# Kernel tuning notes

Hardware: AMD Instinct MI355X
Metric: run time of the kernel (lower is better)

## Reference

```python
import jax, jax.numpy as jnp
import numpy as np

OFFSET = 1
NUM_ENTITY = 128

def setup_inputs() -> dict:
    key = jax.random.key(0)
    ks = jax.random.split(key, 8)
    B, L, D = 32, 2048, 1024
    M, E, S = 256, NUM_ENTITY, 128
    H, P = 2048, 512
    return {
        "sequence_output": jax.random.normal(ks[0], (B, L, D), dtype=jnp.float32),
        "mention_pos": jax.random.randint(ks[1], (B, M), 0, L - 2),
        "mention2entity": jnp.sort(jax.random.randint(ks[2], (B, M), 0, E), axis=-1),
        "sent_pos": jax.random.randint(ks[3], (B, S), 0, L - 2),
        "fc1_w": jax.random.normal(ks[4], (D, H), dtype=jnp.float32) * 0.02,
        "fc1_b": jnp.zeros((H,), dtype=jnp.float32),
        "fc2_w": jax.random.normal(ks[5], (H, P), dtype=jnp.float32) * 0.02,
        "fc2_b": jnp.zeros((P,), dtype=jnp.float32),
    }

def _segment_logsumexp(x, seg):
    # x: [M, D] mention embeddings, seg: [M] entity ids -> [E, D]
    m = jax.ops.segment_max(x, seg, num_segments=NUM_ENTITY)           # [E, D]
    m_safe = jnp.where(jnp.isfinite(m), m, 0.0)
    s = jax.ops.segment_sum(jnp.exp(x - m_safe[seg]), seg, num_segments=NUM_ENTITY)
    cnt = jax.ops.segment_sum(jnp.ones((x.shape[0],), x.dtype), seg, num_segments=NUM_ENTITY)
    s_safe = jnp.where(cnt[:, None] > 0, s, 1.0)
    lse = jnp.log(s_safe) + m_safe
    # entities with no mentions stay zero (torch.zeros init in original)
    return jnp.where(cnt[:, None] > 0, lse, 0.0)

def reference(sequence_output, mention_pos, mention2entity, sent_pos, fc1_w, fc1_b, fc2_w, fc2_b):
    # gather mention start-token states (offset = +1 as in self.offset)
    mention_embed = jnp.take_along_axis(
        sequence_output, (mention_pos + OFFSET)[:, :, None], axis=1)  # [B, M, D]
    sent_embed = jnp.take_along_axis(
        sequence_output, (sent_pos + OFFSET)[:, :, None], axis=1)     # [B, S, D]
    entity_embed = jax.vmap(_segment_logsumexp)(mention_embed, mention2entity)  # [B, E, D]
    nodes = jnp.concatenate([mention_embed, entity_embed, sent_embed], axis=1)  # [B, M+E+S, D]
    # projection(): fc1 then fc2 (no nonlinearity, as in the original)
    h = jnp.einsum('bnd,dh->bnh', nodes, fc1_w) + fc1_b
    return jnp.einsum('bnh,hp->bnp', h, fc2_w) + fc2_b
```

## Files before the change

### kernel.cpp

```cpp
#include <hip/hip_runtime.h>
#include <cstdint>

#define DEV __device__ __forceinline__

typedef __attribute__((ext_vector_type(8))) short short8;
typedef __attribute__((ext_vector_type(4))) float f32x4;

DEV unsigned short f2bf(float f) {
    uint32_t u = __builtin_bit_cast(uint32_t, f);
    u += 0x7fffu + ((u >> 16) & 1u);
    return (unsigned short)(u >> 16);
}

DEV uint32_t cvtpk(float a, float b) {
    uint32_t r;
    asm("v_cvt_pk_bf16_f32 %0, %1, %2" : "=v"(r) : "v"(a), "v"(b));
    return r;
}

DEV uint2 pack4(float4 v) {
    uint2 o;
    o.x = cvtpk(v.x, v.y);
    o.y = cvtpk(v.z, v.w);
    return o;
}

DEV void async_copy16(void* lds, const void* g) {
    __builtin_amdgcn_global_load_lds(
        (const __attribute__((address_space(1))) void*)g,
        (__attribute__((address_space(3))) void*)lds, 16, 0, 0);
}

template <int KLEN, int KSTR, int N>
DEV void gemm_body_part(const unsigned short* __restrict__ A,
                        const unsigned short* __restrict__ Bt,
                        float* __restrict__ P,
                        int Mtot, int rowblk, int colblk, int zidx,
                        unsigned short* Al, unsigned short* Bl) {
    int t = threadIdx.x;
    int lane = t & 63, w = t >> 6;
    int wm = w >> 1, wn = w & 1;
    int row0 = rowblk * 128, col0 = colblk * 128;
    size_t kbase = (size_t)zidx * KLEN;
    f32x4 acc[4][4] = {};

    int rifc = lane >> 2;
    int koff = (lane & 3) * 8;
    int c0 = 2 * w, c1 = 2 * w + 1;

    const unsigned short* Abase = A + (size_t)row0 * KSTR + kbase + koff;
    const unsigned short* Bbase = Bt + (size_t)col0 * KSTR + kbase + koff;

    for (int kt = 0; kt < KLEN / 32; ++kt) {
        int k0 = kt * 32;
        __syncthreads();
        async_copy16(&Al[c0 * 512], Abase + (size_t)(c0 * 16 + rifc) * KSTR + k0);
        async_copy16(&Al[c1 * 512], Abase + (size_t)(c1 * 16 + rifc) * KSTR + k0);
        async_copy16(&Bl[c0 * 512], Bbase + (size_t)(c0 * 16 + rifc) * KSTR + k0);
        async_copy16(&Bl[c1 * 512], Bbase + (size_t)(c1 * 16 + rifc) * KSTR + k0);
        __syncthreads();

        int r = lane & 15, kq = lane >> 4;
        short8 a[4], b[4];
        #pragma unroll
        for (int mi = 0; mi < 4; ++mi)
            a[mi] = *reinterpret_cast<const short8*>(&Al[(wm * 64 + mi * 16 + r) * 32 + kq * 8]);
        #pragma unroll
        for (int ni = 0; ni < 4; ++ni)
            b[ni] = *reinterpret_cast<const short8*>(&Bl[(wn * 64 + ni * 16 + r) * 32 + kq * 8]);
        #pragma unroll
        for (int mi = 0; mi < 4; ++mi)
            #pragma unroll
            for (int ni = 0; ni < 4; ++ni)
                acc[mi][ni] = __builtin_amdgcn_mfma_f32_16x16x32_bf16(a[mi], b[ni], acc[mi][ni], 0, 0, 0);
    }

    int r = lane & 15, kq = lane >> 4;
    float* Pz = P + (size_t)zidx * (size_t)N * (size_t)Mtot;
    #pragma unroll
    for (int mi = 0; mi < 4; ++mi)
        #pragma unroll
        for (int ni = 0; ni < 4; ++ni) {
            int col = col0 + wn * 64 + ni * 16 + r;
            #pragma unroll
            for (int j = 0; j < 4; ++j) {
                int row = row0 + wm * 64 + mi * 16 + kq * 4 + j;
                Pz[(size_t)col * Mtot + row] = acc[mi][ni][j];
            }
        }
}

__global__ __launch_bounds__(256) void k_prep(const float* __restrict__ W1,
                                              const float* __restrict__ W2,
                                              const float* __restrict__ b1,
                                              unsigned short* __restrict__ W1c,
                                              unsigned short* __restrict__ W2t,
                                              float* __restrict__ part) {
    __shared__ unsigned short sh[32][33];
    int blk = blockIdx.x, t = threadIdx.x;
    if (blk < 2048) {
        int i = blk * 256 + t;
        float4 v = reinterpret_cast<const float4*>(W1)[i];
        reinterpret_cast<uint2*>(W1c)[i] = pack4(v);
    } else if (blk < 3072) {
        int idx = blk - 2048;
        int h0 = (idx & 63) * 32, p0 = (idx >> 6) * 32;
        int r = t >> 3, c4 = (t & 7) * 4;
        float4 v = *reinterpret_cast<const float4*>(&W2[(size_t)(h0 + r) * 512 + p0 + c4]);
        sh[r][c4 + 0] = f2bf(v.x);
        sh[r][c4 + 1] = f2bf(v.y);
        sh[r][c4 + 2] = f2bf(v.z);
        sh[r][c4 + 3] = f2bf(v.w);
        __syncthreads();
        uint2 o;
        o.x = (uint32_t)sh[c4 + 0][r] | ((uint32_t)sh[c4 + 1][r] << 16);
        o.y = (uint32_t)sh[c4 + 2][r] | ((uint32_t)sh[c4 + 3][r] << 16);
        *reinterpret_cast<uint2*>(&W2t[(size_t)(p0 + r) * 2048 + h0 + c4]) = o;
    } else {
        int hs = blk - 3072;
        float a0 = 0.f, a1 = 0.f;
        #pragma unroll 4
        for (int hh = 0; hh < 32; ++hh) {
            int h = hs * 32 + hh;
            float bb = b1[h];
            a0 += bb * W2[(size_t)h * 512 + t];
            a1 += bb * W2[(size_t)h * 512 + 256 + t];
        }
        part[hs * 512 + t] = a0;
        part[hs * 512 + 256 + t] = a1;
    }
}

__global__ __launch_bounds__(256) void k_mid(const float* __restrict__ seq,
                                             const int* __restrict__ mpos,
                                             const int* __restrict__ m2e,
                                             const unsigned short* __restrict__ W1c,
                                             const unsigned short* __restrict__ W2t,
                                             float* __restrict__ Wpart,
                                             const float* __restrict__ part,
                                             const float* __restrict__ b2,
                                             float* __restrict__ fb,
                                             unsigned short* __restrict__ ent) {
    __shared__ unsigned short Al[128 * 32];
    __shared__ unsigned short Bl[128 * 32];
    __shared__ int sm[256];
    __shared__ int sp[256];
    __shared__ int slo, shi;
    int blk = blockIdx.x, t = threadIdx.x;
    if (blk < 128) {
        gemm_body_part<512, 2048, 512>(W1c, W2t, Wpart, 1024,
                                       (blk >> 2) & 7, blk & 3, blk >> 5, Al, Bl);
    } else if (blk < 130) {
        int p = (blk - 128) * 256 + t;
        float s = b2[p];
        #pragma unroll
        for (int hs = 0; hs < 64; ++hs) s += part[hs * 512 + p];
        fb[p] = s;
    } else {
        int idx = blk - 130;
        int b = idx >> 7, e = idx & 127;
        sm[t] = m2e[b * 256 + t];
        sp[t] = mpos[b * 256 + t] + 1;
        if (t == 0) { slo = 0; shi = 0; }
        __syncthreads();
        if (sm[t] == e && (t == 0 || sm[t - 1] != e)) slo = t;
        if (sm[t] == e && (t == 255 || sm[t + 1] != e)) shi = t + 1;
        __syncthreads();
        int lo = slo, hi = shi;
        float ox, oy, oz, ow;
        if (hi > lo) {
            float s0 = 0.f, s1 = 0.f, s2 = 0.f, s3 = 0.f;
            for (int j = lo; j < hi; ++j) {
                float4 v = *reinterpret_cast<const float4*>(
                    &seq[((size_t)b * 2048 + sp[j]) * 1024 + t * 4]);
                s0 += __expf(v.x); s1 += __expf(v.y);
                s2 += __expf(v.z); s3 += __expf(v.w);
            }
            ox = __logf(s0); oy = __logf(s1);
            oz = __logf(s2); ow = __logf(s3);
        } else {
            ox = oy = oz = ow = 0.f;
        }
        float4 o; o.x = ox; o.y = oy; o.z = oz; o.w = ow;
        *reinterpret_cast<uint2*>(&ent[((size_t)b * 128 + e) * 1024 + t * 4]) = pack4(o);
    }
}

__global__ __launch_bounds__(256) void k_wreduce(const float* __restrict__ P,
                                                 unsigned short* __restrict__ Wt) {
    const size_t SPLIT = 512u * 1024u;
    int i = blockIdx.x * 256 + threadIdx.x;
    float4 a = reinterpret_cast<const float4*>(P)[i];
    float4 b = reinterpret_cast<const float4*>(P + SPLIT)[i];
    float4 c = reinterpret_cast<const float4*>(P + 2 * SPLIT)[i];
    float4 d = reinterpret_cast<const float4*>(P + 3 * SPLIT)[i];
    float4 s;
    s.x = a.x + b.x + c.x + d.x;
    s.y = a.y + b.y + c.y + d.y;
    s.z = a.z + b.z + c.z + d.z;
    s.w = a.w + b.w + c.w + d.w;
    reinterpret_cast<uint2*>(Wt)[i] = pack4(s);
}

__global__ __launch_bounds__(256) void k_gemm_main(const float* __restrict__ seq,
                                                   const int* __restrict__ mpos,
                                                   const int* __restrict__ spos,
                                                   const unsigned short* __restrict__ ent,
                                                   const unsigned short* __restrict__ Wt,
                                                   float* __restrict__ C,
                                                   const float* __restrict__ fb) {
    __shared__ unsigned short Al[2][128 * 32];
    __shared__ unsigned short Bl[2][128 * 32];
    int p = blockIdx.x;
    int cpx = gridDim.x >> 3;
    int L = (p & 7) * cpx + (p >> 3);
    int colblk = L & 3;
    int rowblk = L >> 2;

    int t = threadIdx.x;
    int lane = t & 63, w = t >> 6;
    int wm = w >> 1, wn = w & 1;
    int row0 = rowblk * 128, col0 = colblk * 128;
    int b = rowblk >> 2, quad = rowblk & 3;
    f32x4 acc[4][4] = {};

    int rifc = lane >> 2;
    int koff = (((lane & 3) ^ (rifc & 3)) * 8);
    int c0 = 2 * w, c1 = 2 * w + 1;
    const unsigned short* Bbase = Wt + (size_t)col0 * 1024 + koff;

    auto compute = [&](const unsigned short* AB, const unsigned short* BB) {
        int r = lane & 15, kq = lane >> 4;
        int sq = (kq ^ (r & 3)) * 8;
        short8 a[4], bfr[4];
        #pragma unroll
        for (int mi = 0; mi < 4; ++mi)
            a[mi] = *reinterpret_cast<const short8*>(&AB[(wm * 64 + mi * 16 + r) * 32 + sq]);
        #pragma unroll
        for (int ni = 0; ni < 4; ++ni)
            bfr[ni] = *reinterpret_cast<const short8*>(&BB[(wn * 64 + ni * 16 + r) * 32 + sq]);
        #pragma unroll
        for (int mi = 0; mi < 4; ++mi)
            #pragma unroll
            for (int ni = 0; ni < 4; ++ni)
                acc[mi][ni] = __builtin_amdgcn_mfma_f32_16x16x32_bf16(a[mi], bfr[ni], acc[mi][ni], 0, 0, 0);
    };

    auto stageB = [&](int kt) {
        int k0 = kt * 64;
        async_copy16(&Bl[0][c0 * 512], Bbase + (size_t)(c0 * 16 + rifc) * 1024 + k0);
        async_copy16(&Bl[0][c1 * 512], Bbase + (size_t)(c1 * 16 + rifc) * 1024 + k0);
        async_copy16(&Bl[1][c0 * 512], Bbase + (size_t)(c0 * 16 + rifc) * 1024 + k0 + 32);
        async_copy16(&Bl[1][c1 * 512], Bbase + (size_t)(c1 * 16 + rifc) * 1024 + k0 + 32);
    };

    if (quad == 2) {
        const unsigned short* Abase = ent + (size_t)b * 128 * 1024 + koff;
        #pragma unroll 1
        for (int kt = 0; kt < 16; ++kt) {
            int k0 = kt * 64;
            __syncthreads();
            async_copy16(&Al[0][c0 * 512], Abase + (size_t)(c0 * 16 + rifc) * 1024 + k0);
            async_copy16(&Al[0][c1 * 512], Abase + (size_t)(c1 * 16 + rifc) * 1024 + k0);
            async_copy16(&Al[1][c0 * 512], Abase + (size_t)(c0 * 16 + rifc) * 1024 + k0 + 32);
            async_copy16(&Al[1][c1 * 512], Abase + (size_t)(c1 * 16 + rifc) * 1024 + k0 + 32);
            stageB(kt);
            __syncthreads();
            compute(Al[0], Bl[0]);
            compute(Al[1], Bl[1]);
        }
    } else {
        int rloc = t >> 3;
        int cof = (t & 7) * 4;
        int wof = ((((t & 7) >> 1) ^ (rloc & 3)) * 8) + ((t & 7) & 1) * 4;
        const float* rp[4];
        {
            int m0, m1, m2, m3;
            if (quad == 3) {
                m0 = spos[b * 128 + rloc] + 1;
                m1 = spos[b * 128 + 32 + rloc] + 1;
                m2 = spos[b * 128 + 64 + rloc] + 1;
                m3 = spos[b * 128 + 96 + rloc] + 1;
            } else {
                int mb = b * 256 + quad * 128;
                m0 = mpos[mb + rloc] + 1;
                m1 = mpos[mb + 32 + rloc] + 1;
                m2 = mpos[mb + 64 + rloc] + 1;
                m3 = mpos[mb + 96 + rloc] + 1;
            }
            rp[0] = seq + ((size_t)b * 2048 + m0) * 1024 + cof;
            rp[1] = seq + ((size_t)b * 2048 + m1) * 1024 + cof;
            rp[2] = seq + ((size_t)b * 2048 + m2) * 1024 + cof;
            rp[3] = seq + ((size_t)b * 2048 + m3) * 1024 + cof;
        }
        float4 va[8], vn[8];
        auto loadA = [&](int kt, float4* dst) {
            int k0 = kt * 64;
            #pragma unroll
            for (int j = 0; j < 4; ++j) {
                dst[j * 2]     = *reinterpret_cast<const float4*>(rp[j] + k0);
                dst[j * 2 + 1] = *reinterpret_cast<const float4*>(rp[j] + k0 + 32);
            }
        };
        auto writeA = [&](const float4* src) {
            #pragma unroll
            for (int j = 0; j < 4; ++j) {
                *reinterpret_cast<uint2*>(&Al[0][(j * 32 + rloc) * 32 + wof]) = pack4(src[j * 2]);
                *reinterpret_cast<uint2*>(&Al[1][(j * 32 + rloc) * 32 + wof]) = pack4(src[j * 2 + 1]);
            }
        };
        loadA(0, va);
        #pragma unroll 1
        for (int kt = 0; kt < 16; ++kt) {
            __syncthreads();
            writeA(va);
            stageB(kt);
            __syncthreads();
            if (kt < 15) loadA(kt + 1, vn);
            compute(Al[0], Bl[0]);
            compute(Al[1], Bl[1]);
            #pragma unroll
            for (int j = 0; j < 8; ++j) va[j] = vn[j];
        }
    }

    int r = lane & 15, kq = lane >> 4;
    #pragma unroll
    for (int mi = 0; mi < 4; ++mi)
        #pragma unroll
        for (int ni = 0; ni < 4; ++ni) {
            int col = col0 + wn * 64 + ni * 16 + r;
            float bv = fb[col];
            #pragma unroll
            for (int j = 0; j < 4; ++j) {
                int row = row0 + wm * 64 + mi * 16 + kq * 4 + j;
                C[(size_t)row * 512 + col] = acc[mi][ni][j] + bv;
            }
        }
}


extern "C" void kernel_launch(void* const* d_in, const int* in_sizes, int n_in,
                              void* d_out, int out_size, void* d_ws, size_t ws_size,
                              hipStream_t stream) {
    const float* seq  = (const float*)d_in[0];
    const int*   mpos = (const int*)d_in[1];
    const int*   m2e  = (const int*)d_in[2];
    const int*   spos = (const int*)d_in[3];
    const float* W1   = (const float*)d_in[4];
    const float* b1   = (const float*)d_in[5];
    const float* W2   = (const float*)d_in[6];
    const float* b2   = (const float*)d_in[7];
    float* out = (float*)d_out;

    char* ws = (char*)d_ws;
    unsigned short* W1c   = (unsigned short*)(ws);
    unsigned short* W2t   = (unsigned short*)(ws + (4u << 20));
    unsigned short* Wt    = (unsigned short*)(ws + (6u << 20));
    float*          Wpart = (float*)(ws + (8u << 20));
    float*          part  = (float*)(ws + (16u << 20));
    float*          fb    = (float*)(ws + (16u << 20) + (1u << 18));
    unsigned short* ent   = (unsigned short*)(ws + (24u << 20));

    k_prep<<<3136, 256, 0, stream>>>(W1, W2, b1, W1c, W2t, part);
    k_mid<<<4226, 256, 0, stream>>>(seq, mpos, m2e, W1c, W2t, Wpart, part, b2, fb, ent);
    k_wreduce<<<512, 256, 0, stream>>>(Wpart, Wt);
    k_gemm_main<<<512, 256, 0, stream>>>(seq, mpos, spos, ent, Wt, out, fb);
}
```

Before: 56.70 us.

## Replace split-K weight product with full-K 64x64 tiles and drop reduce kernel

The fused weight product W1·W2 previously ran as split-K over four slices, writing fp32 partials that a separate kernel summed and converted to bf16. It now uses 64x64 output tiles, each covering the full K range in one block, and writes bf16 directly. This removes one kernel launch and the fp32 partial write/read traffic. In exchange, each GEMM block runs a longer serial K loop with less MFMA work per step, which could lengthen the tail of the mid kernel.

After: 59.89 us. 1.06x slower.

```diff
diff --git a/kernel.cpp b/kernel.cpp
--- a/kernel.cpp
+++ b/kernel.cpp
@@ -29,65 +29,6 @@
     __builtin_amdgcn_global_load_lds(
         (const __attribute__((address_space(1))) void*)g,
         (__attribute__((address_space(3))) void*)lds, 16, 0, 0);
-}
-
-template <int KLEN, int KSTR, int N>
-DEV void gemm_body_part(const unsigned short* __restrict__ A,
-                        const unsigned short* __restrict__ Bt,
-                        float* __restrict__ P,
-                        int Mtot, int rowblk, int colblk, int zidx,
-                        unsigned short* Al, unsigned short* Bl) {
-    int t = threadIdx.x;
-    int lane = t & 63, w = t >> 6;
-    int wm = w >> 1, wn = w & 1;
-    int row0 = rowblk * 128, col0 = colblk * 128;
-    size_t kbase = (size_t)zidx * KLEN;
-    f32x4 acc[4][4] = {};
-
-    int rifc = lane >> 2;
-    int koff = (lane & 3) * 8;
-    int c0 = 2 * w, c1 = 2 * w + 1;
-
-    const unsigned short* Abase = A + (size_t)row0 * KSTR + kbase + koff;
-    const unsigned short* Bbase = Bt + (size_t)col0 * KSTR + kbase + koff;
-
-    for (int kt = 0; kt < KLEN / 32; ++kt) {
-        int k0 = kt * 32;
-        __syncthreads();
-        async_copy16(&Al[c0 * 512], Abase + (size_t)(c0 * 16 + rifc) * KSTR + k0);
-        async_copy16(&Al[c1 * 512], Abase + (size_t)(c1 * 16 + rifc) * KSTR + k0);
-        async_copy16(&Bl[c0 * 512], Bbase + (size_t)(c0 * 16 + rifc) * KSTR + k0);
-        async_copy16(&Bl[c1 * 512], Bbase + (size_t)(c1 * 16 + rifc) * KSTR + k0);
-        __syncthreads();
-
-        int r = lane & 15, kq = lane >> 4;
-        short8 a[4], b[4];
-        #pragma unroll
-        for (int mi = 0; mi < 4; ++mi)
-            a[mi] = *reinterpret_cast<const short8*>(&Al[(wm * 64 + mi * 16 + r) * 32 + kq * 8]);
-        #pragma unroll
-        for (int ni = 0; ni < 4; ++ni)
-            b[ni] = *reinterpret_cast<const short8*>(&Bl[(wn * 64 + ni * 16 + r) * 32 + kq * 8]);
-        #pragma unroll
-        for (int mi = 0; mi < 4; ++mi)
-            #pragma unroll
-            for (int ni = 0; ni < 4; ++ni)
-                acc[mi][ni] = __builtin_amdgcn_mfma_f32_16x16x32_bf16(a[mi], b[ni], acc[mi][ni], 0, 0, 0);
-    }
-
-    int r = lane & 15, kq = lane >> 4;
-    float* Pz = P + (size_t)zidx * (size_t)N * (size_t)Mtot;
-    #pragma unroll
-    for (int mi = 0; mi < 4; ++mi)
-        #pragma unroll
-        for (int ni = 0; ni < 4; ++ni) {
-            int col = col0 + wn * 64 + ni * 16 + r;
-            #pragma unroll
-            for (int j = 0; j < 4; ++j) {
-                int row = row0 + wm * 64 + mi * 16 + kq * 4 + j;
-                Pz[(size_t)col * Mtot + row] = acc[mi][ni][j];
-            }
-        }
 }
 
 __global__ __launch_bounds__(256) void k_prep(const float* __restrict__ W1,
@@ -136,20 +77,68 @@
                                              const int* __restrict__ m2e,
                                              const unsigned short* __restrict__ W1c,
                                              const unsigned short* __restrict__ W2t,
-                                             float* __restrict__ Wpart,
+                                             unsigned short* __restrict__ Wt,
                                              const float* __restrict__ part,
                                              const float* __restrict__ b2,
                                              float* __restrict__ fb,
                                              unsigned short* __restrict__ ent) {
-    __shared__ unsigned short Al[128 * 32];
-    __shared__ unsigned short Bl[128 * 32];
+    __shared__ unsigned short Al[2][64 * 32];
+    __shared__ unsigned short Bl[2][64 * 32];
     __shared__ int sm[256];
     __shared__ int sp[256];
     __shared__ int slo, shi;
     int blk = blockIdx.x, t = threadIdx.x;
     if (blk < 128) {
-        gemm_body_part<512, 2048, 512>(W1c, W2t, Wpart, 1024,
-                                       (blk >> 2) & 7, blk & 3, blk >> 5, Al, Bl);
+        int rowblk = blk >> 3, colblk = blk & 7;
+        int row0 = rowblk * 64, col0 = colblk * 64;
+        int lane = t & 63, w = t >> 6;
+        int wm = w >> 1, wn = w & 1;
+        f32x4 acc[2][2] = {};
+
+        int rifc = lane >> 2;
+        int koff = (lane & 3) * 8;
+        const unsigned short* Abase = W1c + (size_t)(row0 + w * 16 + rifc) * 2048 + koff;
+        const unsigned short* Bbase = W2t + (size_t)(col0 + w * 16 + rifc) * 2048 + koff;
+
+        #pragma unroll 1
+        for (int kt = 0; kt < 32; ++kt) {
+            int k0 = kt * 64;
+            __syncthreads();
+            async_copy16(&Al[0][w * 512], Abase + k0);
+            async_copy16(&Al[1][w * 512], Abase + k0 + 32);
+            async_copy16(&Bl[0][w * 512], Bbase + k0);
+            async_copy16(&Bl[1][w * 512], Bbase + k0 + 32);
+            __syncthreads();
+            int r = lane & 15, kq = lane >> 4;
+            #pragma unroll
+            for (int s = 0; s < 2; ++s) {
+                short8 a[2], b[2];
+                #pragma unroll
+                for (int mi = 0; mi < 2; ++mi)
+                    a[mi] = *reinterpret_cast<const short8*>(&Al[s][(wm * 32 + mi * 16 + r) * 32 + kq * 8]);
+                #pragma unroll
+                for (int ni = 0; ni < 2; ++ni)
+                    b[ni] = *reinterpret_cast<const short8*>(&Bl[s][(wn * 32 + ni * 16 + r) * 32 + kq * 8]);
+                #pragma unroll
+                for (int mi = 0; mi < 2; ++mi)
+                    #pragma unroll
+                    for (int ni = 0; ni < 2; ++ni)
+                        acc[mi][ni] = __builtin_amdgcn_mfma_f32_16x16x32_bf16(a[mi], b[ni], acc[mi][ni], 0, 0, 0);
+            }
+        }
+
+        int r = lane & 15, kq = lane >> 4;
+        #pragma unroll
+        for (int mi = 0; mi < 2; ++mi)
+            #pragma unroll
+            for (int ni = 0; ni < 2; ++ni) {
+                int colp = col0 + wn * 32 + ni * 16 + r;
+                #pragma unroll
+                for (int j = 0; j < 4; ++j) {
+                    int rowd = row0 + wm * 32 + mi * 16 + kq * 4 + j;
+                    Wt[(size_t)colp * 1024 + rowd] = f2bf(acc[mi][ni][j]);
+                }
+            }
     } else if (blk < 130) {
         int p = (blk - 128) * 256 + t;
         float s = b2[p];
@@ -186,22 +175,6 @@
     }
 }
 
-__global__ __launch_bounds__(256) void k_wreduce(const float* __restrict__ P,
-                                                 unsigned short* __restrict__ Wt) {
-    const size_t SPLIT = 512u * 1024u;
-    int i = blockIdx.x * 256 + threadIdx.x;
-    float4 a = reinterpret_cast<const float4*>(P)[i];
-    float4 b = reinterpret_cast<const float4*>(P + SPLIT)[i];
-    float4 c = reinterpret_cast<const float4*>(P + 2 * SPLIT)[i];
-    float4 d = reinterpret_cast<const float4*>(P + 3 * SPLIT)[i];
-    float4 s;
-    s.x = a.x + b.x + c.x + d.x;
-    s.y = a.y + b.y + c.y + d.y;
-    s.z = a.z + b.z + c.z + d.z;
-    s.w = a.w + b.w + c.w + d.w;
-    reinterpret_cast<uint2*>(Wt)[i] = pack4(s);
-}
-
 __global__ __launch_bounds__(256) void k_gemm_main(const float* __restrict__ seq,
                                                    const int* __restrict__ mpos,
                                                    const int* __restrict__ spos,
@@ -357,13 +330,11 @@
     unsigned short* W1c   = (unsigned short*)(ws);
     unsigned short* W2t   = (unsigned short*)(ws + (4u << 20));
     unsigned short* Wt    = (unsigned short*)(ws + (6u << 20));
-    float*          Wpart = (float*)(ws + (8u << 20));
     float*          part  = (float*)(ws + (16u << 20));
     float*          fb    = (float*)(ws + (16u << 20) + (1u << 18));
     unsigned short* ent   = (unsigned short*)(ws + (24u << 20));
 
     k_prep<<<3136, 256, 0, stream>>>(W1, W2, b1, W1c, W2t, part);
-    k_mid<<<4226, 256, 0, stream>>>(seq, mpos, m2e, W1c, W2t, Wpart, part, b2, fb, ent);
-    k_wreduce<<<512, 256, 0, stream>>>(Wpart, Wt);
+    k_mid<<<4226, 256, 0, stream>>>(seq, mpos, m2e, W1c, W2t, Wt, part, b2, fb, ent);
     k_gemm_main<<<512, 256, 0, stream>>>(seq, mpos, spos, ent, Wt, out, fb);
 }
```
